# Kernel tuning notes

Measured on AMD Instinct MI355X. Metric: run time of the kernel, lower is better.

The kernel has to match this reference:

```python
import jax, jax.numpy as jnp
from jax import lax
import numpy as np

SEQ, BATCH, X_DIM = 256, 64, 64
FEAT = 256      # dense_x[-1]
DEC = 256       # dense_h_x[-1]
H = 512         # dim_rnn


def setup_inputs() -> dict:
    key = jax.random.key(0)
    ks = jax.random.split(key, 12)
    s = 0.05
    return {
        "x": jax.random.normal(ks[0], (SEQ, BATCH, X_DIM), jnp.float32),
        "mode_selector": jax.random.uniform(ks[1], (SEQ,), jnp.float32),
        # feature extractor: Linear(x_dim -> FEAT) + tanh
        "W_fx": jax.random.normal(ks[2], (FEAT, X_DIM), jnp.float32) * s,
        "b_fx": jnp.zeros((FEAT,), jnp.float32),
        # LSTM (single layer): gates ordered i, f, g, o (torch convention)
        "W_ih": jax.random.normal(ks[3], (4 * H, FEAT), jnp.float32) * s,
        "W_hh": jax.random.normal(ks[4], (4 * H, H), jnp.float32) * s,
        "b_ih": jnp.zeros((4 * H,), jnp.float32),
        "b_hh": jnp.zeros((4 * H,), jnp.float32),
        # decoder MLP: Linear(H -> DEC) + tanh
        "W_hx": jax.random.normal(ks[5], (DEC, H), jnp.float32) * s,
        "b_hx": jnp.zeros((DEC,), jnp.float32),
        # gen_out: Linear(DEC -> x_dim)
        "W_out": jax.random.normal(ks[6], (X_DIM, DEC), jnp.float32) * s,
        "b_out": jnp.zeros((X_DIM,), jnp.float32),
    }


def _forward(x, mode_selector, W_fx, b_fx, W_ih, W_hh, b_ih, b_hh,
             W_hx, b_hx, W_out, b_out):
    def fe(v):  # feature_extractor_x (dropout_p=0 -> identity)
        return jnp.tanh(v @ W_fx.T + b_fx)

    def gen(h):  # mlp_h_x + gen_out
        return jnp.tanh(h @ W_hx.T + b_hx) @ W_out.T + b_out

    def lstm_cell(feat, h, c):
        g = feat @ W_ih.T + b_ih + h @ W_hh.T + b_hh  # [B, 4H]
        i, f, gg, o = jnp.split(g, 4, axis=-1)
        c2 = jax.nn.sigmoid(f) * c + jax.nn.sigmoid(i) * jnp.tanh(gg)
        h2 = jax.nn.sigmoid(o) * jnp.tanh(c2)
        return h2, c2

    S, B, _ = x.shape
    feat_x = fe(x)  # [S, B, FEAT] teacher-forced features
    h0 = jnp.zeros((B, H), x.dtype)
    c0 = jnp.zeros((B, H), x.dtype)
    y0 = jnp.zeros((B, W_out.shape[0]), x.dtype)

    def step(carry, inp):
        h, c, y_prev = carry
        feat_tf, mix, is_first = inp
        # at t=0 original uses feature_x[0] as the "auto" feature
        feat_auto = jnp.where(is_first, feat_tf, fe(y_prev))
        feat = mix * feat_auto + (1.0 - mix) * feat_tf
        y_t = gen(h)           # generated from pre-update hidden state
        h2, c2 = lstm_cell(feat, h, c)
        return (h2, c2, y_t), y_t

    is_first = (jnp.arange(S) == 0)
    _, y = lax.scan(step, (h0, c0, y0), (feat_x, mode_selector, is_first))
    return y  # [S, B, x_dim]


def reference(x, mode_selector, W_fx, b_fx, W_ih, W_hh, b_ih, b_hh,
              W_hx, b_hx, W_out, b_out):
    return _forward(x, mode_selector, W_fx, b_fx, W_ih, W_hh, b_ih, b_hh,
                    W_hx, b_hx, W_out, b_out)
```

## Files before the change

kernel.cpp:

```cpp
#include <hip/hip_runtime.h>
#include <stdint.h>

typedef unsigned short u16;
typedef unsigned int u32;
typedef unsigned long long u64;
typedef __attribute__((ext_vector_type(8))) short short8;
typedef __attribute__((ext_vector_type(4))) float f32x4;
typedef __attribute__((ext_vector_type(4))) int int4v;

#define SEQ 256
#define GATE_WGS 64
#define D_WGS 8
#define NWG 73
#define A_ELE 49152
#define D_ELE 16384
#define FACC_ELE 16384

__device__ __forceinline__ u16 f2bf(float f) {
  u32 u = __float_as_uint(f);
  u += 0x7FFFu + ((u >> 16) & 1u);
  return (u16)(u >> 16);
}
__device__ __forceinline__ float bf2f(u16 v) {
  return __uint_as_float(((u32)v) << 16);
}
__device__ __forceinline__ short8 cvt8(const float* __restrict__ p) {
  short8 r;
#pragma unroll
  for (int j = 0; j < 8; ++j) r[j] = (short)f2bf(p[j]);
  return r;
}
__device__ __forceinline__ short8 cvt8v(const float* __restrict__ p) {
  f32x4 a = *(const f32x4*)p, b = *(const f32x4*)(p + 4);
  short8 r;
#pragma unroll
  for (int j = 0; j < 4; ++j) { r[j] = (short)f2bf(a[j]); r[4 + j] = (short)f2bf(b[j]); }
  return r;
}
__device__ __forceinline__ float fast_tanh(float x) {
  return 1.0f - 2.0f / (1.0f + __expf(2.0f * x));
}
__device__ __forceinline__ float fast_sig(float x) {
  return 1.0f / (1.0f + __expf(-x));
}

union V16 { short8 s; u64 q[2]; };
__device__ __forceinline__ short8 ldc16(const u16* p) {
  V16 v;
  v.q[0] = __hip_atomic_load((const u64*)p,     __ATOMIC_RELAXED, __HIP_MEMORY_SCOPE_AGENT);
  v.q[1] = __hip_atomic_load((const u64*)p + 1, __ATOMIC_RELAXED, __HIP_MEMORY_SCOPE_AGENT);
  return v.s;
}
__device__ __forceinline__ f32x4 ldc16f(const float* p) {
  union { f32x4 f; u64 q[2]; } v;
  v.q[0] = __hip_atomic_load((const u64*)p,     __ATOMIC_RELAXED, __HIP_MEMORY_SCOPE_AGENT);
  v.q[1] = __hip_atomic_load((const u64*)p + 1, __ATOMIC_RELAXED, __HIP_MEMORY_SCOPE_AGENT);
  return v.f;
}
__device__ __forceinline__ void stc16(u16* p, const u64* s) {
  __hip_atomic_store((u64*)p,     s[0], __ATOMIC_RELAXED, __HIP_MEMORY_SCOPE_AGENT);
  __hip_atomic_store((u64*)p + 1, s[1], __ATOMIC_RELAXED, __HIP_MEMORY_SCOPE_AGENT);
}
__device__ __forceinline__ void atadd(float* p, float v) {
  (void)__hip_atomic_fetch_add(p, v, __ATOMIC_RELAXED, __HIP_MEMORY_SCOPE_AGENT);
}
__device__ __forceinline__ void pollge(u32* p, u32 v) {
  while (__hip_atomic_load(p, __ATOMIC_RELAXED, __HIP_MEMORY_SCOPE_AGENT) < v) {}
}
__device__ __forceinline__ void setflag(u32* p, u32 v) {
  __hip_atomic_store(p, v, __ATOMIC_RELAXED, __HIP_MEMORY_SCOPE_AGENT);
}
#define VMCNT0() asm volatile("s_waitcnt vmcnt(0)" ::: "memory")

__global__ void prep_misc(const float* __restrict__ W_fx, const float* __restrict__ b_fx,
                          const float* __restrict__ W_out, const float* __restrict__ b_out,
                          u16* __restrict__ Abuf0, u32* __restrict__ flags,
                          float* __restrict__ featacc, float* __restrict__ bcomb,
                          u16* __restrict__ Wcpack) {
  int b = blockIdx.x, tid = threadIdx.x;
  if (b == 0) {
    for (int it = 0; it < 16; ++it) {
      int chunk = it * 256 + tid;
      *(int4v*)(Abuf0 + (2048 + chunk) * 8) = (int4v){0, 0, 0, 0};
    }
  } else if (b == 1) {
    for (int k = 0; k < 6; ++k) flags[k * 256 + tid] = 0u;
  } else if (b < 6) {
    float* base = featacc + (b - 2) * 16384;
    for (int it = 0; it < 16; ++it)
      *(f32x4*)(base + (it * 256 + tid) * 4) = (f32x4){0.f, 0.f, 0.f, 0.f};
  } else if (b == 6) {
    float s = b_fx[tid];
    for (int k = 0; k < 64; ++k) s += W_fx[tid * 64 + k] * b_out[k];
    bcomb[tid] = s;
  } else {
    int ct = b - 7;
    for (int it = 0; it < 16; ++it) {
      int o = it * 256 + tid;
      int cl = o >> 8, dec = o & 255;
      int c = ct * 16 + cl;
      float s = 0.f;
      for (int k = 0; k < 64; ++k) s += W_fx[c * 64 + k] * W_out[k * 256 + dec];
      int dwk = dec >> 5, kd = dec & 31;
      int l = (c & 15) + ((kd >> 3) << 4), j = kd & 7;
      Wcpack[((dwk * 16 + (c >> 4)) * 64 + l) * 8 + j] = f2bf(s);
    }
  }
}

__global__ void prep_ftf(const float* __restrict__ x, const float* __restrict__ W_fx,
                         const float* __restrict__ b_fx, u16* __restrict__ ftf) {
  __shared__ __attribute__((aligned(16))) u16 fstage[64 * 264];
  const int t = blockIdx.x, tid = threadIdx.x;
  const int wv = tid >> 6, ln = tid & 63;
  const int c15 = ln & 15, qq = ln >> 4;
  short8 WfR[2][4];
#pragma unroll
  for (int kk = 0; kk < 2; ++kk)
#pragma unroll
    for (int nt = 0; nt < 4; ++nt)
      WfR[kk][nt] = cvt8(W_fx + ((wv * 4 + nt) * 16 + c15) * 64 + kk * 32 + qq * 8);
  float bfx_r[4];
#pragma unroll
  for (int nt = 0; nt < 4; ++nt) bfx_r[nt] = b_fx[(wv * 4 + nt) * 16 + c15];
  short8 xa[2][4];
#pragma unroll
  for (int kb = 0; kb < 2; ++kb)
#pragma unroll
    for (int mt = 0; mt < 4; ++mt)
      xa[kb][mt] = cvt8v(x + (t * 64 + mt * 16 + c15) * 64 + kb * 32 + qq * 8);
  f32x4 tf[4][4];
#pragma unroll
  for (int nt = 0; nt < 4; ++nt)
#pragma unroll
    for (int mt = 0; mt < 4; ++mt) tf[nt][mt] = (f32x4){0.f, 0.f, 0.f, 0.f};
#pragma unroll
  for (int kb = 0; kb < 2; ++kb)
#pragma unroll
    for (int nt = 0; nt < 4; ++nt)
#pragma unroll
      for (int mt = 0; mt < 4; ++mt)
        tf[nt][mt] = __builtin_amdgcn_mfma_f32_16x16x32_bf16(xa[kb][mt], WfR[kb][nt], tf[nt][mt], 0, 0, 0);
#pragma unroll
  for (int nt = 0; nt < 4; ++nt)
#pragma unroll
    for (int mt = 0; mt < 4; ++mt)
#pragma unroll
      for (int r2 = 0; r2 < 4; ++r2) {
        int row = mt * 16 + qq * 4 + r2;
        fstage[row * 264 + (wv * 4 + nt) * 16 + c15] = f2bf(fast_tanh(tf[nt][mt][r2] + bfx_r[nt]));
      }
  __syncthreads();
  u16* ftfb = ftf + t * 16384;
#pragma unroll
  for (int it = 0; it < 8; ++it) {
    int chunk = it * 256 + tid;
    int kb = chunk >> 8, l = chunk & 63;
    int m = ((chunk >> 6) & 3) * 16 + (l & 15);
    int k = kb * 32 + (l >> 4) * 8;
    *(short8*)(ftfb + chunk * 8) = *(const short8*)(fstage + m * 264 + k);
  }
}

__global__ void __launch_bounds__(256, 1)
rnn_kernel(const float* __restrict__ x, const float* __restrict__ msel,
           const float* __restrict__ W_ih, const float* __restrict__ W_hh,
           const float* __restrict__ b_ih, const float* __restrict__ b_hh,
           const float* __restrict__ W_hx, const float* __restrict__ b_hx,
           const float* __restrict__ W_out, const float* __restrict__ b_out,
           float* __restrict__ out,
           u16* __restrict__ Abase, u16* __restrict__ dbase,
           u32* __restrict__ flags, float* __restrict__ featacc,
           const float* __restrict__ bcomb, const u16* __restrict__ Wcpack,
           const u16* __restrict__ ftf, u16* __restrict__ fblend) {
  __shared__ __attribute__((aligned(16))) char smem[109568];
  const int wgid = blockIdx.x;
  const int tid = threadIdx.x;
  const int wv = tid >> 6, ln = tid & 63;
  u32* dflag = flags + 1024;
  u32* hcnt  = flags + 1168;
  u32* fcnt  = flags + 1232;
  u32* fbcnt = flags + 1296;

  if (wgid < GATE_WGS) {
    const int wg = wgid;
    float* red = (float*)smem;
    u16* hstage = (u16*)(smem + 32768);
    short8 Breg[6][2];
#pragma unroll
    for (int kk = 0; kk < 6; ++kk) {
      int kb = wv + kk * 4;
#pragma unroll
      for (int nt = 0; nt < 2; ++nt) {
        int n = ln & 15, q = ln >> 4;
        int gate = nt * 2 + (n >> 3), unit = n & 7;
        int row = gate * 512 + wg * 8 + unit;
        int k = kb * 32 + q * 8;
        const float* src = (k < 256) ? (W_ih + row * 256 + k) : (W_hh + row * 512 + (k - 256));
        Breg[kk][nt] = cvt8(src);
      }
    }
    float bsum_r[2][4];
#pragma unroll
    for (int it = 0; it < 2; ++it) {
      int u = (it * 256 + tid) & 7;
#pragma unroll
      for (int g = 0; g < 4; ++g) {
        int row = g * 512 + wg * 8 + u;
        bsum_r[it][g] = b_ih[row] + b_hh[row];
      }
    }
    float creg[2] = {0.f, 0.f};
    const int kbW = 8 + (wg >> 2), qW = wg & 3;
    int r = 0, rn = 1;
    for (int t = 0; t < SEQ; ++t) {
      if (tid < 4) pollge(&hcnt[tid * 16], (u32)(16 * t));
      else if (tid == 64 && t > 0)
        pollge(&fbcnt[(t & 1) * 16], 8u * ((u32)(t + 1) >> 1));
      __syncthreads();
      const u16* A = Abase + r * A_ELE;
      u16* An = Abase + rn * A_ELE;
      short8 a[6][4];
#pragma unroll
      for (int kk = 2; kk < 6; ++kk) {
        int kb = wv + kk * 4;
#pragma unroll
        for (int mt = 0; mt < 4; ++mt)
          a[kk][mt] = ldc16(A + ((kb * 4 + mt) * 64 + ln) * 8);
      }
      {
        const u16* fsrc = (t == 0) ? ftf : (fblend + (t & 1) * 16384);
#pragma unroll
        for (int kk = 0; kk < 2; ++kk) {
          int kb = wv + kk * 4;
#pragma unroll
          for (int mt = 0; mt < 4; ++mt)
            a[kk][mt] = ldc16(fsrc + ((kb * 4 + mt) * 64 + ln) * 8);
        }
      }
      f32x4 acc[2][4];
#pragma unroll
      for (int nt = 0; nt < 2; nt++)
#pragma unroll
        for (int mt = 0; mt < 4; mt++) acc[nt][mt] = (f32x4){0.f, 0.f, 0.f, 0.f};
#pragma unroll
      for (int kk = 0; kk < 6; ++kk)
#pragma unroll
        for (int nt = 0; nt < 2; nt++)
#pragma unroll
          for (int mt = 0; mt < 4; mt++)
            acc[nt][mt] = __builtin_amdgcn_mfma_f32_16x16x32_bf16(a[kk][mt], Breg[kk][nt], acc[nt][mt], 0, 0, 0);
#pragma unroll
      for (int nt = 0; nt < 2; nt++)
#pragma unroll
        for (int mt = 0; mt < 4; mt++)
          *(f32x4*)(red + ((wv * 8 + nt * 4 + mt) * 64 + ln) * 4) = acc[nt][mt];
      __syncthreads();
#pragma unroll
      for (int it = 0; it < 2; ++it) {
        int item = it * 256 + tid;
        int m = item >> 3, u = item & 7;
        int mt = m >> 4, lq = ((m & 15) >> 2) * 16, reg = m & 3;
        float g4[4];
#pragma unroll
        for (int g = 0; g < 4; ++g) {
          float s = bsum_r[it][g];
          int base = ((g >> 1) * 4 + mt) * 64 + lq + (g & 1) * 8 + u;
#pragma unroll
          for (int w = 0; w < 4; ++w) s += red[(w * 8 * 64 + base) * 4 + reg];
          g4[g] = s;
        }
        float ii = fast_sig(g4[0]), ff = fast_sig(g4[1]);
        float gg = fast_tanh(g4[2]), oo = fast_sig(g4[3]);
        float cn = ff * creg[it] + ii * gg;
        creg[it] = cn;
        float h = oo * fast_tanh(cn);
        hstage[(mt * 16 + (m & 15)) * 8 + u] = f2bf(h);
      }
      __syncthreads();
      if (tid < 64) {
        int mt2 = tid >> 4, m15 = tid & 15;
        u16* dst = An + (((kbW * 4 + mt2) * 64 + qW * 16 + m15) * 8);
        stc16(dst, (const u64*)(hstage + tid * 8));
        VMCNT0();
        if (tid == 0)
          (void)__hip_atomic_fetch_add(&hcnt[(wg & 3) * 16], 1u,
                                       __ATOMIC_RELAXED, __HIP_MEMORY_SCOPE_AGENT);
      }
      r = rn; rn = (rn == 2) ? 0 : rn + 1;
    }
  } else if (wgid < GATE_WGS + D_WGS) {
    const int dw = wgid - GATE_WGS;
    float* red = (float*)smem;
    u16* dstage = (u16*)(smem + 32768);
    short8 Breg[4][2];
#pragma unroll
    for (int kk = 0; kk < 4; ++kk) {
      int kbh = wv * 4 + kk;
#pragma unroll
      for (int nt = 0; nt < 2; ++nt) {
        int n = ln & 15, q = ln >> 4;
        int row = dw * 32 + nt * 16 + n;
        int k = kbh * 32 + q * 8;
        Breg[kk][nt] = cvt8(W_hx + row * 512 + k);
      }
    }
    short8 WcB[4];
#pragma unroll
    for (int nt = 0; nt < 4; ++nt)
      WcB[nt] = *(const short8*)(Wcpack + ((dw * 16 + wv * 4 + nt) * 64 + ln) * 8);
    float bias_r[8];
#pragma unroll
    for (int it = 0; it < 8; ++it) bias_r[it] = b_hx[dw * 32 + ((it * 256 + tid) & 31)];
    const int ci = dw * 256 + tid;
    const int cbase = (ci >> 8) * 32 + ((ci & 63) >> 4) * 8;
    f32x4 bc0 = *(const f32x4*)(bcomb + cbase);
    f32x4 bc1 = *(const f32x4*)(bcomb + cbase + 4);
    int r = 0, rn = 1;
    for (int t = 0; t < SEQ; ++t) {
      if (tid < 4) pollge(&hcnt[tid * 16], (u32)(16 * t));
      __syncthreads();
      const u16* A = Abase + r * A_ELE;
      u16* dbufR = dbase + (t & 1) * D_ELE;
      short8 a[4][4];
#pragma unroll
      for (int kk = 0; kk < 4; ++kk)
#pragma unroll
        for (int mt = 0; mt < 4; ++mt)
          a[kk][mt] = ldc16(A + (((8 + wv * 4 + kk) * 4 + mt) * 64 + ln) * 8);
      f32x4 acc[2][4];
#pragma unroll
      for (int nt = 0; nt < 2; nt++)
#pragma unroll
        for (int mt = 0; mt < 4; mt++) acc[nt][mt] = (f32x4){0.f, 0.f, 0.f, 0.f};
#pragma unroll
      for (int kk = 0; kk < 4; ++kk)
#pragma unroll
        for (int nt = 0; nt < 2; nt++)
#pragma unroll
          for (int mt = 0; mt < 4; mt++)
            acc[nt][mt] = __builtin_amdgcn_mfma_f32_16x16x32_bf16(a[kk][mt], Breg[kk][nt], acc[nt][mt], 0, 0, 0);
#pragma unroll
      for (int nt = 0; nt < 2; nt++)
#pragma unroll
        for (int mt = 0; mt < 4; mt++)
          *(f32x4*)(red + ((wv * 8 + nt * 4 + mt) * 64 + ln) * 4) = acc[nt][mt];
      __syncthreads();
#pragma unroll
      for (int it = 0; it < 8; ++it) {
        int item = it * 256 + tid;
        int m = item >> 5, c = item & 31;
        int mt = m >> 4, lq = ((m & 15) >> 2) * 16, reg = m & 3;
        float s = bias_r[it];
        int base = ((c >> 4) * 4 + mt) * 64 + lq + (c & 15);
#pragma unroll
        for (int w = 0; w < 4; ++w) s += red[(w * 8 * 64 + base) * 4 + reg];
        dstage[((mt * 4 + (c >> 3)) * 16 + (m & 15)) * 8 + (c & 7)] = f2bf(fast_tanh(s));
      }
      __syncthreads();
      stc16(dbufR + (dw * 256 + tid) * 8, (const u64*)(dstage + tid * 8));
      short8 ad[4];
#pragma unroll
      for (int mt = 0; mt < 4; ++mt)
        ad[mt] = *(const short8*)(dstage + ((mt * 4 + (ln >> 4)) * 16 + (ln & 15)) * 8);
      f32x4 pacc[4][4];
#pragma unroll
      for (int nt = 0; nt < 4; ++nt)
#pragma unroll
        for (int mt = 0; mt < 4; ++mt) pacc[nt][mt] = (f32x4){0.f, 0.f, 0.f, 0.f};
#pragma unroll
      for (int nt = 0; nt < 4; ++nt)
#pragma unroll
        for (int mt = 0; mt < 4; ++mt)
          pacc[nt][mt] = __builtin_amdgcn_mfma_f32_16x16x32_bf16(ad[mt], WcB[nt], pacc[nt][mt], 0, 0, 0);
      {
        float* fs = featacc + (t & 3) * FACC_ELE;
#pragma unroll
        for (int nt = 0; nt < 4; ++nt) {
          int c = (wv * 4 + nt) * 16 + (ln & 15);
          int cb = (c >> 5) * 2048 + ((c & 31) >> 3) * 128 + (c & 7);
#pragma unroll
          for (int mt = 0; mt < 4; ++mt)
#pragma unroll
            for (int reg = 0; reg < 4; ++reg)
              atadd(fs + cb + mt * 512 + ((ln >> 4) * 4 + reg) * 8, pacc[nt][mt][reg]);
        }
      }
      VMCNT0();
      __syncthreads();
      if (tid == 0) {
        setflag(&dflag[dw * 16], (u32)(t + 1));
        (void)__hip_atomic_fetch_add(&fcnt[(t & 3) * 16], 1u,
                                     __ATOMIC_RELAXED, __HIP_MEMORY_SCOPE_AGENT);
      }
      if (t < SEQ - 1) {
        if (tid == 0) pollge(&fcnt[(t & 3) * 16], 8u * (((u32)t >> 2) + 1u));
        __syncthreads();
        float* fs = featacc + (t & 3) * FACC_ELE;
        f32x4 lo = ldc16f(fs + ci * 8);
        f32x4 hi = ldc16f(fs + ci * 8 + 4);
        short8 tfv = *(const short8*)(ftf + (t + 1) * 16384 + ci * 8);
        float mixg = msel[t + 1];
        VMCNT0();
        short8 rr;
#pragma unroll
        for (int j = 0; j < 8; ++j) {
          float av = ((j < 4) ? lo[j] : hi[j - 4]) + ((j < 4) ? bc0[j] : bc1[j - 4]);
          float fv = mixg * fast_tanh(av) + (1.f - mixg) * bf2f((u16)tfv[j]);
          rr[j] = (short)f2bf(fv);
        }
        V16 v; v.s = rr;
        stc16(fblend + ((t + 1) & 1) * 16384 + ci * 8, v.q);
        u64 zq[2] = {0ull, 0ull};
        stc16((u16*)(fs + ci * 8), zq);
        stc16((u16*)(fs + ci * 8 + 4), zq);
        VMCNT0();
        __syncthreads();
        if (tid == 0)
          (void)__hip_atomic_fetch_add(&fbcnt[((t + 1) & 1) * 16], 1u,
                                       __ATOMIC_RELAXED, __HIP_MEMORY_SCOPE_AGENT);
      }
      r = rn; rn = (rn == 2) ? 0 : rn + 1;
    }
  } else {
    float* red = (float*)smem;
    const int c15 = ln & 15, qq = ln >> 4;
    short8 WoR[2][4];
#pragma unroll
    for (int kk = 0; kk < 2; ++kk) {
      int koffo = (wv * 2 + kk) * 32 + qq * 8;
#pragma unroll
      for (int nt = 0; nt < 4; ++nt)
        WoR[kk][nt] = cvt8(W_out + (nt * 16 + c15) * 256 + koffo);
    }
    float bout_r = b_out[wv * 16 + c15];
    for (int t = 0; t < SEQ; ++t) {
      if (tid < 8) pollge(&dflag[tid * 16], (u32)(t + 1));
      __syncthreads();
      const u16* dbufR = dbase + (t & 1) * D_ELE;
      short8 da[2][4];
#pragma unroll
      for (int kk = 0; kk < 2; ++kk)
#pragma unroll
        for (int mt = 0; mt < 4; ++mt)
          da[kk][mt] = ldc16(dbufR + (((wv * 2 + kk) * 4 + mt) * 64 + ln) * 8);
      f32x4 acc[4][4];
#pragma unroll
      for (int nt = 0; nt < 4; nt++)
#pragma unroll
        for (int mt = 0; mt < 4; mt++) acc[nt][mt] = (f32x4){0.f, 0.f, 0.f, 0.f};
#pragma unroll
      for (int kk = 0; kk < 2; ++kk)
#pragma unroll
        for (int nt = 0; nt < 4; nt++)
#pragma unroll
          for (int mt = 0; mt < 4; mt++)
            acc[nt][mt] = __builtin_amdgcn_mfma_f32_16x16x32_bf16(da[kk][mt], WoR[kk][nt], acc[nt][mt], 0, 0, 0);
#pragma unroll
      for (int nt = 0; nt < 4; nt++)
#pragma unroll
        for (int mt = 0; mt < 4; mt++)
          *(f32x4*)(red + ((wv * 16 + nt * 4 + mt) * 64 + ln) * 4) = acc[nt][mt];
      __syncthreads();
#pragma unroll
      for (int mt = 0; mt < 4; ++mt) {
        f32x4 s = (f32x4){0.f, 0.f, 0.f, 0.f};
#pragma unroll
        for (int w2 = 0; w2 < 4; ++w2)
          s += *(const f32x4*)(red + ((w2 * 16 + wv * 4 + mt) * 64 + ln) * 4);
#pragma unroll
        for (int r2 = 0; r2 < 4; ++r2) {
          int row = mt * 16 + qq * 4 + r2;
          out[t * 4096 + row * 64 + wv * 16 + c15] = s[r2] + bout_r;
        }
      }
      __syncthreads();
    }
  }
}

extern "C" void kernel_launch(void* const* d_in, const int* in_sizes, int n_in,
                              void* d_out, int out_size, void* d_ws, size_t ws_size,
                              hipStream_t stream) {
  const float* x     = (const float*)d_in[0];
  const float* msel  = (const float*)d_in[1];
  const float* W_fx  = (const float*)d_in[2];
  const float* b_fx  = (const float*)d_in[3];
  const float* W_ih  = (const float*)d_in[4];
  const float* W_hh  = (const float*)d_in[5];
  const float* b_ih  = (const float*)d_in[6];
  const float* b_hh  = (const float*)d_in[7];
  const float* W_hx  = (const float*)d_in[8];
  const float* b_hx  = (const float*)d_in[9];
  const float* W_out = (const float*)d_in[10];
  const float* b_out = (const float*)d_in[11];

  uint8_t* ws = (uint8_t*)d_ws;
  u16*   Abase   = (u16*)ws;
  u16*   dbase   = (u16*)(ws + 294912);
  u32*   flags   = (u32*)(ws + 360448);
  float* featacc = (float*)(ws + 366592);
  float* bcomb   = (float*)(ws + 628736);
  u16*   Wcpack  = (u16*)(ws + 629760);
  u16*   fblend  = (u16*)(ws + 760832);
  u16*   ftf     = (u16*)(ws + 826368);

  prep_misc<<<23, 256, 0, stream>>>(W_fx, b_fx, W_out, b_out,
                                    Abase, flags, featacc, bcomb, Wcpack);
  prep_ftf<<<256, 256, 0, stream>>>(x, W_fx, b_fx, ftf);
  rnn_kernel<<<NWG, 256, 0, stream>>>(x, msel, W_ih, W_hh, b_ih, b_hh,
                                      W_hx, b_hx, W_out, b_out,
                                      (float*)d_out, Abase, dbase, flags,
                                      featacc, bcomb, Wcpack, ftf, fblend);
}
```

Before: 2.581 ms.

## Replace atomic-add feature reduction with shared decoder buffer and per-WG full-K GEMM

The decoder workgroups no longer compute partial feature products and scatter them with float atomic adds into a global accumulator that later has to be zeroed. Each decoder WG now publishes its slice of the decoder activations, waits on a single counter until all eight slices exist, reads the full activation from global memory and computes its own 32 feature columns over the full K in registers. The result is staged through LDS for the tanh/blend step. The decoder buffer becomes four-deep and the per-WG flags are merged into one shared counter. This removes the 16K-element atomic traffic and the zeroing stores, at the cost of an extra all-to-all barrier and global reads on the serial critical path.

New measurement: 2.270 ms. 1.14x faster.

```diff
diff --git a/kernel.cpp b/kernel.cpp
--- a/kernel.cpp
+++ b/kernel.cpp
@@ -14,7 +14,6 @@
 #define NWG 73
 #define A_ELE 49152
 #define D_ELE 16384
-#define FACC_ELE 16384
 
 __device__ __forceinline__ u16 f2bf(float f) {
   u32 u = __float_as_uint(f);
@@ -51,19 +50,10 @@
   v.q[1] = __hip_atomic_load((const u64*)p + 1, __ATOMIC_RELAXED, __HIP_MEMORY_SCOPE_AGENT);
   return v.s;
 }
-__device__ __forceinline__ f32x4 ldc16f(const float* p) {
-  union { f32x4 f; u64 q[2]; } v;
-  v.q[0] = __hip_atomic_load((const u64*)p,     __ATOMIC_RELAXED, __HIP_MEMORY_SCOPE_AGENT);
-  v.q[1] = __hip_atomic_load((const u64*)p + 1, __ATOMIC_RELAXED, __HIP_MEMORY_SCOPE_AGENT);
-  return v.f;
-}
 __device__ __forceinline__ void stc16(u16* p, const u64* s) {
   __hip_atomic_store((u64*)p,     s[0], __ATOMIC_RELAXED, __HIP_MEMORY_SCOPE_AGENT);
   __hip_atomic_store((u64*)p + 1, s[1], __ATOMIC_RELAXED, __HIP_MEMORY_SCOPE_AGENT);
 }
-__device__ __forceinline__ void atadd(float* p, float v) {
-  (void)__hip_atomic_fetch_add(p, v, __ATOMIC_RELAXED, __HIP_MEMORY_SCOPE_AGENT);
-}
 __device__ __forceinline__ void pollge(u32* p, u32 v) {
   while (__hip_atomic_load(p, __ATOMIC_RELAXED, __HIP_MEMORY_SCOPE_AGENT) < v) {}
 }
@@ -75,8 +65,7 @@
 __global__ void prep_misc(const float* __restrict__ W_fx, const float* __restrict__ b_fx,
                           const float* __restrict__ W_out, const float* __restrict__ b_out,
                           u16* __restrict__ Abuf0, u32* __restrict__ flags,
-                          float* __restrict__ featacc, float* __restrict__ bcomb,
-                          u16* __restrict__ Wcpack) {
+                          float* __restrict__ bcomb, u16* __restrict__ Wcpack) {
   int b = blockIdx.x, tid = threadIdx.x;
   if (b == 0) {
     for (int it = 0; it < 16; ++it) {
@@ -85,16 +74,12 @@
     }
   } else if (b == 1) {
     for (int k = 0; k < 6; ++k) flags[k * 256 + tid] = 0u;
-  } else if (b < 6) {
-    float* base = featacc + (b - 2) * 16384;
-    for (int it = 0; it < 16; ++it)
-      *(f32x4*)(base + (it * 256 + tid) * 4) = (f32x4){0.f, 0.f, 0.f, 0.f};
-  } else if (b == 6) {
+  } else if (b == 2) {
     float s = b_fx[tid];
     for (int k = 0; k < 64; ++k) s += W_fx[tid * 64 + k] * b_out[k];
     bcomb[tid] = s;
   } else {
-    int ct = b - 7;
+    int ct = b - 3;
     for (int it = 0; it < 16; ++it) {
       int o = it * 256 + tid;
       int cl = o >> 8, dec = o & 255;
@@ -170,16 +155,15 @@
            const float* __restrict__ W_out, const float* __restrict__ b_out,
            float* __restrict__ out,
            u16* __restrict__ Abase, u16* __restrict__ dbase,
-           u32* __restrict__ flags, float* __restrict__ featacc,
+           u32* __restrict__ flags,
            const float* __restrict__ bcomb, const u16* __restrict__ Wcpack,
            const u16* __restrict__ ftf, u16* __restrict__ fblend) {
   __shared__ __attribute__((aligned(16))) char smem[109568];
   const int wgid = blockIdx.x;
   const int tid = threadIdx.x;
   const int wv = tid >> 6, ln = tid & 63;
-  u32* dflag = flags + 1024;
   u32* hcnt  = flags + 1168;
-  u32* fcnt  = flags + 1232;
+  u32* dcnt  = flags + 1232;
   u32* fbcnt = flags + 1296;
 
   if (wgid < GATE_WGS) {
@@ -293,6 +277,7 @@
     const int dw = wgid - GATE_WGS;
     float* red = (float*)smem;
     u16* dstage = (u16*)(smem + 32768);
+    float* fstg = (float*)(smem + 36864);
     short8 Breg[4][2];
 #pragma unroll
     for (int kk = 0; kk < 4; ++kk) {
@@ -305,23 +290,26 @@
         Breg[kk][nt] = cvt8(W_hx + row * 512 + k);
       }
     }
-    short8 WcB[4];
-#pragma unroll
-    for (int nt = 0; nt < 4; ++nt)
-      WcB[nt] = *(const short8*)(Wcpack + ((dw * 16 + wv * 4 + nt) * 64 + ln) * 8);
+    short8 WcB[8][2];
+#pragma unroll
+    for (int kb = 0; kb < 8; ++kb)
+#pragma unroll
+      for (int ntl = 0; ntl < 2; ++ntl)
+        WcB[kb][ntl] = *(const short8*)(Wcpack + ((kb * 16 + dw * 2 + ntl) * 64 + ln) * 8);
     float bias_r[8];
 #pragma unroll
     for (int it = 0; it < 8; ++it) bias_r[it] = b_hx[dw * 32 + ((it * 256 + tid) & 31)];
     const int ci = dw * 256 + tid;
-    const int cbase = (ci >> 8) * 32 + ((ci & 63) >> 4) * 8;
-    f32x4 bc0 = *(const f32x4*)(bcomb + cbase);
-    f32x4 bc1 = *(const f32x4*)(bcomb + cbase + 4);
+    const int m_bl = ((tid >> 6) & 3) * 16 + (tid & 15);
+    const int cl0 = ((tid & 63) >> 4) * 8;
+    f32x4 bc0 = *(const f32x4*)(bcomb + dw * 32 + cl0);
+    f32x4 bc1 = *(const f32x4*)(bcomb + dw * 32 + cl0 + 4);
     int r = 0, rn = 1;
     for (int t = 0; t < SEQ; ++t) {
       if (tid < 4) pollge(&hcnt[tid * 16], (u32)(16 * t));
       __syncthreads();
       const u16* A = Abase + r * A_ELE;
-      u16* dbufR = dbase + (t & 1) * D_ELE;
+      u16* dbufR = dbase + (t & 3) * D_ELE;
       short8 a[4][4];
 #pragma unroll
       for (int kk = 0; kk < 4; ++kk)
@@ -359,61 +347,56 @@
       }
       __syncthreads();
       stc16(dbufR + (dw * 256 + tid) * 8, (const u64*)(dstage + tid * 8));
-      short8 ad[4];
-#pragma unroll
-      for (int mt = 0; mt < 4; ++mt)
-        ad[mt] = *(const short8*)(dstage + ((mt * 4 + (ln >> 4)) * 16 + (ln & 15)) * 8);
-      f32x4 pacc[4][4];
-#pragma unroll
-      for (int nt = 0; nt < 4; ++nt)
-#pragma unroll
-        for (int mt = 0; mt < 4; ++mt) pacc[nt][mt] = (f32x4){0.f, 0.f, 0.f, 0.f};
-#pragma unroll
-      for (int nt = 0; nt < 4; ++nt)
-#pragma unroll
-        for (int mt = 0; mt < 4; ++mt)
-          pacc[nt][mt] = __builtin_amdgcn_mfma_f32_16x16x32_bf16(ad[mt], WcB[nt], pacc[nt][mt], 0, 0, 0);
-      {
-        float* fs = featacc + (t & 3) * FACC_ELE;
-#pragma unroll
-        for (int nt = 0; nt < 4; ++nt) {
-          int c = (wv * 4 + nt) * 16 + (ln & 15);
-          int cb = (c >> 5) * 2048 + ((c & 31) >> 3) * 128 + (c & 7);
+      VMCNT0();
+      __syncthreads();
+      if (tid == 0)
+        (void)__hip_atomic_fetch_add(dcnt, 1u, __ATOMIC_RELAXED, __HIP_MEMORY_SCOPE_AGENT);
+      if (t < SEQ - 1) {
+        if (tid == 0) pollge(dcnt, 8u * (u32)(t + 1));
+        __syncthreads();
+        f32x4 pacc[2][4];
+#pragma unroll
+        for (int ntl = 0; ntl < 2; ++ntl)
+#pragma unroll
+          for (int mt = 0; mt < 4; ++mt) pacc[ntl][mt] = (f32x4){0.f, 0.f, 0.f, 0.f};
+#pragma unroll
+        for (int half = 0; half < 2; ++half) {
+          short8 a2[4][4];
+#pragma unroll
+          for (int k2 = 0; k2 < 4; ++k2)
+#pragma unroll
+            for (int mt = 0; mt < 4; ++mt)
+              a2[k2][mt] = ldc16(dbufR + (((half * 4 + k2) * 4 + mt) * 64 + ln) * 8);
+#pragma unroll
+          for (int k2 = 0; k2 < 4; ++k2)
+#pragma unroll
+            for (int ntl = 0; ntl < 2; ++ntl)
+#pragma unroll
+              for (int mt = 0; mt < 4; ++mt)
+                pacc[ntl][mt] = __builtin_amdgcn_mfma_f32_16x16x32_bf16(a2[k2][mt], WcB[half * 4 + k2][ntl], pacc[ntl][mt], 0, 0, 0);
+        }
+#pragma unroll
+        for (int ntl = 0; ntl < 2; ++ntl)
 #pragma unroll
           for (int mt = 0; mt < 4; ++mt)
 #pragma unroll
-            for (int reg = 0; reg < 4; ++reg)
-              atadd(fs + cb + mt * 512 + ((ln >> 4) * 4 + reg) * 8, pacc[nt][mt][reg]);
-        }
-      }
-      VMCNT0();
-      __syncthreads();
-      if (tid == 0) {
-        setflag(&dflag[dw * 16], (u32)(t + 1));
-        (void)__hip_atomic_fetch_add(&fcnt[(t & 3) * 16], 1u,
-                                     __ATOMIC_RELAXED, __HIP_MEMORY_SCOPE_AGENT);
-      }
-      if (t < SEQ - 1) {
-        if (tid == 0) pollge(&fcnt[(t & 3) * 16], 8u * (((u32)t >> 2) + 1u));
+            for (int reg = 0; reg < 4; ++reg) {
+              int m = mt * 16 + (ln >> 4) * 4 + reg;
+              int cl = ntl * 16 + (ln & 15);
+              fstg[m * 32 + cl] = pacc[ntl][mt][reg];
+            }
         __syncthreads();
-        float* fs = featacc + (t & 3) * FACC_ELE;
-        f32x4 lo = ldc16f(fs + ci * 8);
-        f32x4 hi = ldc16f(fs + ci * 8 + 4);
+        float mixg = msel[t + 1];
         short8 tfv = *(const short8*)(ftf + (t + 1) * 16384 + ci * 8);
-        float mixg = msel[t + 1];
-        VMCNT0();
         short8 rr;
 #pragma unroll
         for (int j = 0; j < 8; ++j) {
-          float av = ((j < 4) ? lo[j] : hi[j - 4]) + ((j < 4) ? bc0[j] : bc1[j - 4]);
+          float av = fstg[m_bl * 32 + cl0 + j] + ((j < 4) ? bc0[j] : bc1[j - 4]);
           float fv = mixg * fast_tanh(av) + (1.f - mixg) * bf2f((u16)tfv[j]);
           rr[j] = (short)f2bf(fv);
         }
         V16 v; v.s = rr;
         stc16(fblend + ((t + 1) & 1) * 16384 + ci * 8, v.q);
-        u64 zq[2] = {0ull, 0ull};
-        stc16((u16*)(fs + ci * 8), zq);
-        stc16((u16*)(fs + ci * 8 + 4), zq);
         VMCNT0();
         __syncthreads();
         if (tid == 0)
@@ -435,9 +418,9 @@
     }
     float bout_r = b_out[wv * 16 + c15];
     for (int t = 0; t < SEQ; ++t) {
-      if (tid < 8) pollge(&dflag[tid * 16], (u32)(t + 1));
-      __syncthreads();
-      const u16* dbufR = dbase + (t & 1) * D_ELE;
+      if (tid == 0) pollge(dcnt, 8u * (u32)(t + 1));
+      __syncthreads();
+      const u16* dbufR = dbase + (t & 3) * D_ELE;
       short8 da[2][4];
 #pragma unroll
       for (int kk = 0; kk < 2; ++kk)
@@ -496,20 +479,19 @@
   const float* b_out = (const float*)d_in[11];
 
   uint8_t* ws = (uint8_t*)d_ws;
-  u16*   Abase   = (u16*)ws;
-  u16*   dbase   = (u16*)(ws + 294912);
-  u32*   flags   = (u32*)(ws + 360448);
-  float* featacc = (float*)(ws + 366592);
-  float* bcomb   = (float*)(ws + 628736);
-  u16*   Wcpack  = (u16*)(ws + 629760);
-  u16*   fblend  = (u16*)(ws + 760832);
-  u16*   ftf     = (u16*)(ws + 826368);
-
-  prep_misc<<<23, 256, 0, stream>>>(W_fx, b_fx, W_out, b_out,
-                                    Abase, flags, featacc, bcomb, Wcpack);
+  u16*   Abase  = (u16*)ws;
+  u16*   dbase  = (u16*)(ws + 294912);
+  u32*   flags  = (u32*)(ws + 425984);
+  float* bcomb  = (float*)(ws + 432128);
+  u16*   Wcpack = (u16*)(ws + 433152);
+  u16*   fblend = (u16*)(ws + 564224);
+  u16*   ftf    = (u16*)(ws + 629760);
+
+  prep_misc<<<19, 256, 0, stream>>>(W_fx, b_fx, W_out, b_out,
+                                    Abase, flags, bcomb, Wcpack);
   prep_ftf<<<256, 256, 0, stream>>>(x, W_fx, b_fx, ftf);
   rnn_kernel<<<NWG, 256, 0, stream>>>(x, msel, W_ih, W_hh, b_ih, b_hh,
                                       W_hx, b_hx, W_out, b_out,
                                       (float*)d_out, Abase, dbase, flags,
-                                      featacc, bcomb, Wcpack, ftf, fblend);
-}
+                                      bcomb, Wcpack, ftf, fblend);
+}
```
